# Performance work log

Measured on AMD Instinct MI355X. Metric: run time of the kernel, lower is better.

## Reference

```python
import jax, jax.numpy as jnp
import numpy as np

B, S, D = 2, 2048, 1024
H, HKV, HD = 16, 4, 64
FF = 4096
WINDOW = 1024
EPS = 1e-6


def _rope_tables(seq_len, head_dim, base=10000.0):
    inv_freq = 1.0 / (base ** (np.arange(0, head_dim, 2, dtype=np.float32) / head_dim))
    t = np.arange(seq_len, dtype=np.float32)
    freqs = np.outer(t, inv_freq)                       # [S, HD/2]
    emb = np.concatenate([freqs, freqs], axis=-1)       # [S, HD]
    return jnp.asarray(np.cos(emb)), jnp.asarray(np.sin(emb))


def setup_inputs() -> dict:
    key = jax.random.key(0)
    ks = jax.random.split(key, 16)
    s = lambda fan: 1.0 / np.sqrt(fan)
    cos, sin = _rope_tables(S, HD)
    return {
        "hidden_states": jax.random.normal(ks[0], (B, S, D), jnp.float32),
        "cos": cos, "sin": sin,
        "wq": jax.random.normal(ks[1], (D, H * HD), jnp.float32) * s(D),
        "bq": jnp.zeros((H * HD,), jnp.float32),
        "wk": jax.random.normal(ks[2], (D, HKV * HD), jnp.float32) * s(D),
        "bk": jnp.zeros((HKV * HD,), jnp.float32),
        "wv": jax.random.normal(ks[3], (D, HKV * HD), jnp.float32) * s(D),
        "bv": jnp.zeros((HKV * HD,), jnp.float32),
        "wo": jax.random.normal(ks[4], (H * HD, D), jnp.float32) * s(H * HD),
        "ln1_w": jnp.ones((D,), jnp.float32),
        "ln2_w": jnp.ones((D,), jnp.float32),
        "w_gate": jax.random.normal(ks[5], (D, FF), jnp.float32) * s(D),
        "w_up": jax.random.normal(ks[6], (D, FF), jnp.float32) * s(D),
        "w_down": jax.random.normal(ks[7], (FF, D), jnp.float32) * s(FF),
    }


def _rmsnorm(x, w, eps=EPS):
    var = jnp.mean(x.astype(jnp.float32) ** 2, axis=-1, keepdims=True)
    return (x * jax.lax.rsqrt(var + eps)).astype(x.dtype) * w


def _rotate_half(x):
    x1, x2 = jnp.split(x, 2, axis=-1)
    return jnp.concatenate([-x2, x1], axis=-1)


def reference(hidden_states, cos, sin, wq, bq, wk, bk, wv, bv, wo,
              ln1_w, ln2_w, w_gate, w_up, w_down):
    residual = hidden_states
    h = _rmsnorm(hidden_states, ln1_w)

    # projections -> [B, S, H, HD]
    q = (h @ wq + bq).reshape(B, S, H, HD)
    k = (h @ wk + bk).reshape(B, S, HKV, HD)
    v = (h @ wv + bv).reshape(B, S, HKV, HD)

    # RoPE
    c = cos[None, :, None, :]
    sn = sin[None, :, None, :]
    q = q * c + _rotate_half(q) * sn
    k = k * c + _rotate_half(k) * sn

    # GQA: repeat KV heads to H heads
    groups = H // HKV
    k = jnp.repeat(k, groups, axis=2)  # [B, S, H, HD]
    v = jnp.repeat(v, groups, axis=2)

    # sliding-window causal attention (flex_attention block-mask semantics)
    scale = 1.0 / np.sqrt(HD)
    scores = jnp.einsum("bqhd,bkhd->bhqk", q, k) * scale  # [B, H, S, S]
    i = jnp.arange(S)[:, None]
    j = jnp.arange(S)[None, :]
    mask = (j <= i) & (i - j < WINDOW)
    scores = jnp.where(mask[None, None], scores, jnp.finfo(scores.dtype).min)
    attn = jax.nn.softmax(scores, axis=-1)
    ctx = jnp.einsum("bhqk,bkhd->bqhd", attn, v).reshape(B, S, H * HD)

    h = residual + ctx @ wo

    residual2 = h
    h2 = _rmsnorm(h, ln2_w)
    mlp = (jax.nn.silu(h2 @ w_gate) * (h2 @ w_up)) @ w_down
    return residual2 + mlp
```

## Files before the change

### kernel.cpp

```cpp
#include <hip/hip_runtime.h>
#include <hip/hip_bf16.h>
#include <hip/hip_fp16.h>
#include <math.h>

#define BB 2
#define SS 2048
#define DD 1024
#define HH 16
#define HKVN 4
#define HDIM 64
#define FFD 4096
#define WND 1024
#define EPSF 1e-6f

typedef _Float16 f16;
typedef _Float16 half8 __attribute__((ext_vector_type(8)));
typedef float f32x4 __attribute__((ext_vector_type(4)));
typedef unsigned int u32;

#define GLOAD_LDS(gp, lp)                                                  \
  __builtin_amdgcn_global_load_lds(                                        \
      (const __attribute__((address_space(1))) u32*)(gp),                  \
      (__attribute__((address_space(3))) u32*)(lp), 16, 0, 0)

static __device__ inline u32 pack2(float a, float b) {
  unsigned short ua = __builtin_bit_cast(unsigned short, (f16)a);
  unsigned short ub = __builtin_bit_cast(unsigned short, (f16)b);
  return (u32)ua | ((u32)ub << 16);
}

__global__ __launch_bounds__(256) void prep_weights_kernel(
    const float* __restrict__ wq, const float* __restrict__ wk,
    const float* __restrict__ wv, const float* __restrict__ wo,
    const float* __restrict__ wg, const float* __restrict__ wu,
    const float* __restrict__ wd, const float* __restrict__ bq,
    const float* __restrict__ bk, const float* __restrict__ bv,
    f16* __restrict__ qkvT, f16* __restrict__ woT, f16* __restrict__ wgT,
    f16* __restrict__ wuT, f16* __restrict__ wdT, float* __restrict__ biasC) {
  int t = blockIdx.x;
  if (t >= 3712) {
    int i = (t - 3712) * 256 + threadIdx.x;
    if (i < 1024)
      biasC[i] = bq[i];
    else if (i < 1280)
      biasC[i] = bk[i - 1024];
    else if (i < 1536)
      biasC[i] = bv[i - 1280];
    return;
  }
  const float* W;
  f16* Wt;
  int K, N, lt;
  if (t < 256) {
    W = wq; Wt = qkvT; K = 1024; N = 1024; lt = t;
  } else if (t < 320) {
    W = wk; Wt = qkvT + (size_t)1024 * 1024; K = 1024; N = 256; lt = t - 256;
  } else if (t < 384) {
    W = wv; Wt = qkvT + (size_t)1280 * 1024; K = 1024; N = 256; lt = t - 320;
  } else if (t < 640) {
    W = wo; Wt = woT; K = 1024; N = 1024; lt = t - 384;
  } else if (t < 1664) {
    W = wg; Wt = wgT; K = 1024; N = 4096; lt = t - 640;
  } else if (t < 2688) {
    W = wu; Wt = wuT; K = 1024; N = 4096; lt = t - 1664;
  } else {
    W = wd; Wt = wdT; K = 4096; N = 1024; lt = t - 2688;
  }
  int ntx = N >> 6;
  int n0 = (lt % ntx) * 64, k0 = (lt / ntx) * 64;
  __shared__ float tile[64][65];
  int tx = threadIdx.x & 63, tr = threadIdx.x >> 6;
#pragma unroll
  for (int i = 0; i < 16; i++) {
    int r = tr + i * 4;
    tile[r][tx] = W[(size_t)(k0 + r) * N + n0 + tx];
  }
  __syncthreads();
  int kx = (threadIdx.x & 31) * 2;
  int rr = threadIdx.x >> 5;
#pragma unroll
  for (int i = 0; i < 8; i++) {
    int r = rr + i * 8;
    u32 w = pack2(tile[kx][r], tile[kx + 1][r]);
    *(u32*)(Wt + (size_t)(n0 + r) * K + k0 + kx) = w;
  }
}

__global__ __launch_bounds__(256) void rmsnorm_kernel(
    const float* __restrict__ x, const float* __restrict__ w,
    f16* __restrict__ out) {
  int row = blockIdx.x;
  int tid = threadIdx.x;
  float4 v = ((const float4*)(x + (size_t)row * 1024))[tid];
  float ss = v.x * v.x + v.y * v.y + v.z * v.z + v.w * v.w;
  for (int o = 32; o > 0; o >>= 1) ss += __shfl_down(ss, o, 64);
  __shared__ float red[4];
  int wid = tid >> 6, lane = tid & 63;
  if (lane == 0) red[wid] = ss;
  __syncthreads();
  if (tid == 0)
    red[0] = rsqrtf((red[0] + red[1] + red[2] + red[3]) / 1024.f + EPSF);
  __syncthreads();
  float rs = red[0];
  float4 wv = ((const float4*)w)[tid];
  u32 lo = pack2(v.x * rs * wv.x, v.y * rs * wv.y);
  u32 hi = pack2(v.z * rs * wv.z, v.w * rs * wv.w);
  *(int2*)(out + (size_t)row * 1024 + tid * 4) = make_int2((int)lo, (int)hi);
}

__global__ __launch_bounds__(256) void qkv_gemm(
    const f16* __restrict__ A, const f16* __restrict__ Bt,
    const float* __restrict__ biasC, const float* __restrict__ cos_t,
    const float* __restrict__ sin_t, f16* __restrict__ Qh,
    f16* __restrict__ Kh, f16* __restrict__ Vh, int M, int N, int K) {
  __shared__ __align__(16) char smem[3 * 16384];
  const int tid = threadIdx.x;
  const int lane = tid & 63;
  const int wid = tid >> 6;
  const int wr = wid >> 1, wc = wid & 1;
  const int row0 = blockIdx.y * 128, col0 = blockIdx.x * 128;

  f32x4 acc[4][4];
#pragma unroll
  for (int m = 0; m < 4; m++)
#pragma unroll
    for (int n = 0; n < 4; n++) acc[m][n] = (f32x4){0.f, 0.f, 0.f, 0.f};

  auto stage = [&](int buf, int k0) {
    char* base = smem + buf * 16384;
#pragma unroll
    for (int q = 0; q < 2; q++) {
      int s = wid * 128 + q * 64 + lane;
      int r = s >> 2;
      int cg = (s & 3) ^ ((r >> 1) & 3);
      size_t goff = (size_t)r * K + k0 + cg * 8;
      u32 ldsb = (u32)((wid * 2 + q) * 1024);
      GLOAD_LDS(A + (size_t)row0 * K + goff, base + ldsb);
      GLOAD_LDS(Bt + (size_t)col0 * K + goff, base + 8192 + ldsb);
    }
  };
  auto off = [&](int r, int g) -> int {
    return r * 64 + ((g ^ ((r >> 1) & 3)) << 4);
  };

  const int nt = K / 32;
  stage(0, 0);
  if (nt > 1) stage(1, 32);
  int cur = 0;
  const int g = lane >> 4, l15 = lane & 15;
  for (int t = 0; t < nt; t++) {
    if (t + 1 < nt)
      asm volatile("s_waitcnt vmcnt(4)" ::: "memory");
    else
      asm volatile("s_waitcnt vmcnt(0)" ::: "memory");
    asm volatile("s_waitcnt lgkmcnt(0)" ::: "memory");
    __builtin_amdgcn_sched_barrier(0);
    __builtin_amdgcn_s_barrier();
    __builtin_amdgcn_sched_barrier(0);
    const char* base = smem + cur * 16384;
    half8 af[4], bf[4];
#pragma unroll
    for (int m = 0; m < 4; m++) {
      int r = wr * 64 + m * 16 + l15;
      af[m] = *(const half8*)(base + off(r, g));
    }
#pragma unroll
    for (int n = 0; n < 4; n++) {
      int c = wc * 64 + n * 16 + l15;
      bf[n] = *(const half8*)(base + 8192 + off(c, g));
    }
    if (t + 2 < nt) {
      int nb = cur + 2;
      if (nb >= 3) nb -= 3;
      stage(nb, (t + 2) * 32);
    }
    __builtin_amdgcn_s_setprio(1);
#pragma unroll
    for (int m = 0; m < 4; m++)
#pragma unroll
      for (int n = 0; n < 4; n++)
        acc[m][n] =
            __builtin_amdgcn_mfma_f32_16x16x32_f16(af[m], bf[n], acc[m][n], 0, 0, 0);
    __builtin_amdgcn_s_setprio(0);
    cur = (cur + 1 == 3) ? 0 : cur + 1;
  }

  const int typ = (col0 < 1024) ? 0 : (col0 < 1280 ? 1 : 2);
#pragma unroll
  for (int m = 0; m < 4; m++) {
#pragma unroll
    for (int v = 0; v < 4; v++) {
      int r = row0 + wr * 64 + m * 16 + (lane >> 4) * 4 + v;
      int s = r & (SS - 1);
      if (typ == 2) {
#pragma unroll
        for (int n = 0; n < 4; n++) {
          int c = col0 + wc * 64 + n * 16 + l15;
          float vv = acc[m][n][v] + biasC[c];
          Vh[(size_t)r * 256 + (c - 1280)] = (f16)vv;
        }
      } else {
#pragma unroll
        for (int n = 0; n < 2; n++) {
          int d = n * 16 + l15;
          int c1 = col0 + wc * 64 + d;
          float x1 = acc[m][n][v] + biasC[c1];
          float x2 = acc[m][n + 2][v] + biasC[c1 + 32];
          float cv = cos_t[s * HDIM + d];
          float sv = sin_t[s * HDIM + d];
          float o1 = x1 * cv - x2 * sv;
          float o2 = x2 * cv + x1 * sv;
          if (typ == 0) {
            int h = c1 >> 6;
            f16* qp = Qh + ((size_t)r * HH + h) * HDIM + d;
            qp[0] = (f16)(o1 * 0.125f);
            qp[32] = (f16)(o2 * 0.125f);
          } else {
            int hk = (c1 - 1024) >> 6;
            f16* kp = Kh + ((size_t)r * HKVN + hk) * HDIM + d;
            kp[0] = (f16)o1;
            kp[32] = (f16)o2;
          }
        }
      }
    }
  }
}

__global__ __launch_bounds__(256) void gemm_n64(
    const f16* __restrict__ A, const f16* __restrict__ Bt,
    const float* __restrict__ resid, float* __restrict__ Cf, int M, int N,
    int K) {
  __shared__ __align__(16) char smem[3 * 12288];
  const int tid = threadIdx.x;
  const int lane = tid & 63;
  const int wid = tid >> 6;
  const int wr = wid >> 1, wc = wid & 1;
  const int row0 = blockIdx.y * 128, col0 = blockIdx.x * 64;

  f32x4 acc[4][2];
#pragma unroll
  for (int m = 0; m < 4; m++)
#pragma unroll
    for (int n = 0; n < 2; n++) acc[m][n] = (f32x4){0.f, 0.f, 0.f, 0.f};

  auto stage = [&](int buf, int k0) {
    char* base = smem + buf * 12288;
#pragma unroll
    for (int p = 0; p < 2; p++) {
      int s = p * 256 + tid;
      int r = s >> 2;
      int cg = (s & 3) ^ ((r >> 1) & 3);
      size_t goff = (size_t)r * K + k0 + cg * 8;
      GLOAD_LDS(A + (size_t)row0 * K + goff, base + p * 4096 + wid * 1024);
    }
    {
      int s = tid;
      int r = s >> 2;
      int cg = (s & 3) ^ ((r >> 1) & 3);
      size_t goff = (size_t)r * K + k0 + cg * 8;
      GLOAD_LDS(Bt + (size_t)col0 * K + goff, base + 8192 + wid * 1024);
    }
  };
  auto off = [&](int r, int g) -> int {
    return r * 64 + ((g ^ ((r >> 1) & 3)) << 4);
  };

  const int nt = K / 32;
  stage(0, 0);
  if (nt > 1) stage(1, 32);
  int cur = 0;
  const int g = lane >> 4, l15 = lane & 15;
  for (int t = 0; t < nt; t++) {
    if (t + 1 < nt)
      asm volatile("s_waitcnt vmcnt(3)" ::: "memory");
    else
      asm volatile("s_waitcnt vmcnt(0)" ::: "memory");
    asm volatile("s_waitcnt lgkmcnt(0)" ::: "memory");
    __builtin_amdgcn_sched_barrier(0);
    __builtin_amdgcn_s_barrier();
    __builtin_amdgcn_sched_barrier(0);
    const char* base = smem + cur * 12288;
    half8 af[4], bf[2];
#pragma unroll
    for (int m = 0; m < 4; m++) {
      int r = wr * 64 + m * 16 + l15;
      af[m] = *(const half8*)(base + off(r, g));
    }
#pragma unroll
    for (int n = 0; n < 2; n++) {
      int c = wc * 32 + n * 16 + l15;
      bf[n] = *(const half8*)(base + 8192 + off(c, g));
    }
    if (t + 2 < nt) {
      int nb = cur + 2;
      if (nb >= 3) nb -= 3;
      stage(nb, (t + 2) * 32);
    }
    __builtin_amdgcn_s_setprio(1);
#pragma unroll
    for (int m = 0; m < 4; m++)
#pragma unroll
      for (int n = 0; n < 2; n++)
        acc[m][n] =
            __builtin_amdgcn_mfma_f32_16x16x32_f16(af[m], bf[n], acc[m][n], 0, 0, 0);
    __builtin_amdgcn_s_setprio(0);
    cur = (cur + 1 == 3) ? 0 : cur + 1;
  }

#pragma unroll
  for (int m = 0; m < 4; m++) {
#pragma unroll
    for (int n = 0; n < 2; n++) {
#pragma unroll
      for (int v = 0; v < 4; v++) {
        int r = row0 + wr * 64 + m * 16 + (lane >> 4) * 4 + v;
        int c = col0 + wc * 32 + n * 16 + l15;
        float vv = acc[m][n][v] + resid[(size_t)r * N + c];
        Cf[(size_t)r * N + c] = vv;
      }
    }
  }
}

__global__ __launch_bounds__(512) void gateup_gemm(
    const f16* __restrict__ A, const f16* __restrict__ Wg,
    const f16* __restrict__ Wu, f16* __restrict__ ACT, int M, int N, int K) {
  __shared__ __align__(16) char smem[3 * 40960];
  const int tid = threadIdx.x;
  const int lane = tid & 63;
  const int wid = tid >> 6;
  const int wr = wid >> 2;
  const int wc = wid & 3;
  const int row0 = blockIdx.y * 128, col0 = blockIdx.x * 256;

  f32x4 accg[4][4], accu[4][4];
#pragma unroll
  for (int m = 0; m < 4; m++)
#pragma unroll
    for (int n = 0; n < 4; n++) {
      accg[m][n] = (f32x4){0.f, 0.f, 0.f, 0.f};
      accu[m][n] = (f32x4){0.f, 0.f, 0.f, 0.f};
    }

  auto stage = [&](int buf, int k0) {
    char* base = smem + buf * 40960;
    {
      int s = tid;
      int r = s >> 2;
      int cg = (s & 3) ^ ((r >> 1) & 3);
      size_t goff = (size_t)r * K + k0 + cg * 8;
      GLOAD_LDS(A + (size_t)row0 * K + goff, base + wid * 1024);
    }
#pragma unroll
    for (int p = 0; p < 2; p++) {
      int s = p * 512 + tid;
      int r = s >> 2;
      int cg = (s & 3) ^ ((r >> 1) & 3);
      size_t goff = (size_t)r * K + k0 + cg * 8;
      GLOAD_LDS(Wg + (size_t)col0 * K + goff,
                base + 8192 + p * 8192 + wid * 1024);
    }
#pragma unroll
    for (int p = 0; p < 2; p++) {
      int s = p * 512 + tid;
      int r = s >> 2;
      int cg = (s & 3) ^ ((r >> 1) & 3);
      size_t goff = (size_t)r * K + k0 + cg * 8;
      GLOAD_LDS(Wu + (size_t)col0 * K + goff,
                base + 24576 + p * 8192 + wid * 1024);
    }
  };
  auto off = [&](int r, int g) -> int {
    return r * 64 + ((g ^ ((r >> 1) & 3)) << 4);
  };

  const int nt = K / 32;
  stage(0, 0);
  if (nt > 1) stage(1, 32);
  int cur = 0;
  const int g = lane >> 4, l15 = lane & 15;
  for (int t = 0; t < nt; t++) {
    if (t + 1 < nt)
      asm volatile("s_waitcnt vmcnt(5)" ::: "memory");
    else
      asm volatile("s_waitcnt vmcnt(0)" ::: "memory");
    asm volatile("s_waitcnt lgkmcnt(0)" ::: "memory");
    __builtin_amdgcn_sched_barrier(0);
    __builtin_amdgcn_s_barrier();
    __builtin_amdgcn_sched_barrier(0);
    const char* base = smem + cur * 40960;
    half8 af[4], gf[4], uf[4];
#pragma unroll
    for (int m = 0; m < 4; m++) {
      int r = wr * 64 + m * 16 + l15;
      af[m] = *(const half8*)(base + off(r, g));
    }
#pragma unroll
    for (int n = 0; n < 4; n++) {
      int c = wc * 64 + n * 16 + l15;
      gf[n] = *(const half8*)(base + 8192 + off(c, g));
      uf[n] = *(const half8*)(base + 24576 + off(c, g));
    }
    if (t + 2 < nt) {
      int nb = cur + 2;
      if (nb >= 3) nb -= 3;
      stage(nb, (t + 2) * 32);
    }
    __builtin_amdgcn_s_setprio(1);
#pragma unroll
    for (int m = 0; m < 4; m++)
#pragma unroll
      for (int n = 0; n < 4; n++) {
        accg[m][n] =
            __builtin_amdgcn_mfma_f32_16x16x32_f16(af[m], gf[n], accg[m][n], 0, 0, 0);
        accu[m][n] =
            __builtin_amdgcn_mfma_f32_16x16x32_f16(af[m], uf[n], accu[m][n], 0, 0, 0);
      }
    __builtin_amdgcn_s_setprio(0);
    cur = (cur + 1 == 3) ? 0 : cur + 1;
  }

#pragma unroll
  for (int m = 0; m < 4; m++) {
#pragma unroll
    for (int n = 0; n < 4; n++) {
#pragma unroll
      for (int v = 0; v < 4; v++) {
        int r = row0 + wr * 64 + m * 16 + (lane >> 4) * 4 + v;
        int c = col0 + wc * 64 + n * 16 + l15;
        float gg = accg[m][n][v];
        float uu = accu[m][n][v];
        float sv = gg / (1.f + __expf(-gg));
        ACT[(size_t)r * N + c] = (f16)(sv * uu);
      }
    }
  }
}

__global__ __launch_bounds__(256) void vtrans_kernel(
    const f16* __restrict__ Vh, f16* __restrict__ Vt) {
  __shared__ f16 tile[64][72];
  int st = blockIdx.x & 31;
  int hk = (blockIdx.x >> 5) & 3;
  int b = blockIdx.x >> 7;
  int s0 = st * 64;
  int tid = threadIdx.x;
  int r = tid >> 2, cg = tid & 3;
#pragma unroll
  for (int i = 0; i < 2; i++) {
    const f16* src =
        Vh + (size_t)(b * SS + s0 + r) * 256 + hk * HDIM + cg * 16 + i * 8;
    *(int4*)&tile[r][cg * 16 + i * 8] = *(const int4*)src;
  }
  __syncthreads();
  int dd = tid >> 2, sg = tid & 3;
#pragma unroll
  for (int i = 0; i < 4; i++) {
    int c0 = sg * 16 + i * 4;
    unsigned short a0 = __builtin_bit_cast(unsigned short, tile[c0 + 0][dd]);
    unsigned short a1 = __builtin_bit_cast(unsigned short, tile[c0 + 1][dd]);
    unsigned short a2 = __builtin_bit_cast(unsigned short, tile[c0 + 2][dd]);
    unsigned short a3 = __builtin_bit_cast(unsigned short, tile[c0 + 3][dd]);
    u32 w0 = (u32)a0 | ((u32)a1 << 16);
    u32 w1 = (u32)a2 | ((u32)a3 << 16);
    *(int2*)(Vt + ((size_t)(b * HKVN + hk) * HDIM + dd) * SS + s0 + c0) =
        make_int2((int)w0, (int)w1);
  }
}

__global__ __launch_bounds__(256) void attn_kernel(
    const f16* __restrict__ Qh, const f16* __restrict__ Kh,
    const f16* __restrict__ Vt, f16* __restrict__ O) {
  __shared__ __align__(16) char smem[2 * 16384 + 4 * 4608];
  const int tid = threadIdx.x;
  const int lane = tid & 63;
  const int wid = tid >> 6;
  const int l15 = lane & 15;
  const int g = lane >> 4;
  int qt = blockIdx.x & 63;
  int hk = (blockIdx.x >> 6) & 3;
  int b = blockIdx.x >> 8;
  int s0 = qt * 32;
  int h = hk * 4 + wid;

  half8 qf[2][2];
#pragma unroll
  for (int n = 0; n < 2; n++) {
    int q = s0 + n * 16 + l15;
    const f16* qp = Qh + (((size_t)b * SS + q) * HH + h) * HDIM;
#pragma unroll
    for (int kk = 0; kk < 2; kk++) qf[n][kk] = *(const half8*)(qp + kk * 32 + g * 8);
  }

  const int tb = (s0 >= WND) ? ((s0 - (WND - 1)) >> 6) : 0;
  const int te = (s0 + 31) >> 6;

  f32x4 acc_o[2][4];
#pragma unroll
  for (int m2 = 0; m2 < 2; m2++)
#pragma unroll
    for (int n = 0; n < 4; n++) acc_o[m2][n] = (f32x4){0.f, 0.f, 0.f, 0.f};
  float mrun[2] = {-1e30f, -1e30f};
  float lrun[2] = {0.f, 0.f};

  char* pw = smem + 32768 + wid * 4608;

  auto stage = [&](int buf, int tt) {
    int jt0 = tt * 64;
    char* kbase = smem + buf * 16384;
#pragma unroll
    for (int q2 = 0; q2 < 2; q2++) {
      int slot = (wid * 2 + q2) * 64 + lane;
      int r = slot >> 3, c = slot & 7;
      int cc = c ^ (r & 7);
      u32 ldsb = (u32)((wid * 2 + q2) * 1024);
      const f16* gk =
          Kh + ((size_t)(b * SS + jt0 + r) * HKVN + hk) * HDIM + cc * 8;
      GLOAD_LDS(gk, kbase + ldsb);
      const f16* gv =
          Vt + ((size_t)(b * HKVN + hk) * HDIM + r) * SS + jt0 + cc * 8;
      GLOAD_LDS(gv, kbase + 8192 + ldsb);
    }
  };

  stage(0, tb);
  __syncthreads();
  for (int tt = tb; tt <= te; tt++) {
    int buf = (tt - tb) & 1;
    if (tt < te) stage(buf ^ 1, tt + 1);
    const char* kb = smem + buf * 16384;
    const char* vbp = kb + 8192;
    int jt0 = tt * 64;

    f32x4 acc_s[4][2];
#pragma unroll
    for (int m = 0; m < 4; m++)
#pragma unroll
      for (int n = 0; n < 2; n++) acc_s[m][n] = (f32x4){0.f, 0.f, 0.f, 0.f};
#pragma unroll
    for (int kk = 0; kk < 2; kk++) {
      half8 af[4];
#pragma unroll
      for (int m = 0; m < 4; m++) {
        int key = m * 16 + l15;
        af[m] = *(const half8*)(kb + key * 128 + (((kk * 4 + g) ^ (key & 7)) << 4));
      }
#pragma unroll
      for (int m = 0; m < 4; m++)
#pragma unroll
        for (int n = 0; n < 2; n++)
          acc_s[m][n] = __builtin_amdgcn_mfma_f32_16x16x32_f16(af[m], qf[n][kk],
                                                               acc_s[m][n], 0, 0, 0);
    }

    float tmax[2] = {-1e38f, -1e38f};
#pragma unroll
    for (int m = 0; m < 4; m++)
#pragma unroll
      for (int n = 0; n < 2; n++)
#pragma unroll
        for (int v = 0; v < 4; v++) {
          int j = jt0 + m * 16 + g * 4 + v;
          int q = s0 + n * 16 + l15;
          float s = acc_s[m][n][v];
          s = ((unsigned)(q - j) < (unsigned)WND) ? s : -1e38f;
          acc_s[m][n][v] = s;
          tmax[n] = fmaxf(tmax[n], s);
        }
#pragma unroll
    for (int n = 0; n < 2; n++) {
      tmax[n] = fmaxf(tmax[n], __shfl_xor(tmax[n], 16, 64));
      tmax[n] = fmaxf(tmax[n], __shfl_xor(tmax[n], 32, 64));
    }
    float corr[2], rs[2];
#pragma unroll
    for (int n = 0; n < 2; n++) {
      float mn = fmaxf(mrun[n], tmax[n]);
      corr[n] = __expf(mrun[n] - mn);
      mrun[n] = mn;
      rs[n] = 0.f;
    }
#pragma unroll
    for (int m = 0; m < 4; m++)
#pragma unroll
      for (int n = 0; n < 2; n++) {
        float p0 = __expf(acc_s[m][n][0] - mrun[n]);
        float p1 = __expf(acc_s[m][n][1] - mrun[n]);
        float p2 = __expf(acc_s[m][n][2] - mrun[n]);
        float p3 = __expf(acc_s[m][n][3] - mrun[n]);
        rs[n] += (p0 + p1) + (p2 + p3);
        *(int2*)(pw + (n * 16 + l15) * 144 + (m * 16 + g * 4) * 2) =
            make_int2((int)pack2(p0, p1), (int)pack2(p2, p3));
      }
#pragma unroll
    for (int n = 0; n < 2; n++) {
      rs[n] += __shfl_xor(rs[n], 16, 64);
      rs[n] += __shfl_xor(rs[n], 32, 64);
      lrun[n] = lrun[n] * corr[n] + rs[n];
    }
#pragma unroll
    for (int m2 = 0; m2 < 2; m2++)
#pragma unroll
      for (int v = 0; v < 4; v++) {
        float cw = __shfl(corr[m2], g * 4 + v, 64);
#pragma unroll
        for (int n = 0; n < 4; n++) acc_o[m2][n][v] *= cw;
      }
#pragma unroll
    for (int kk = 0; kk < 2; kk++) {
      half8 ap[2], vf[4];
#pragma unroll
      for (int m2 = 0; m2 < 2; m2++)
        ap[m2] = *(const half8*)(pw + (m2 * 16 + l15) * 144 + (kk * 32 + g * 8) * 2);
#pragma unroll
      for (int n = 0; n < 4; n++) {
        int d = n * 16 + l15;
        vf[n] = *(const half8*)(vbp + d * 128 + (((kk * 4 + g) ^ (d & 7)) << 4));
      }
#pragma unroll
      for (int m2 = 0; m2 < 2; m2++)
#pragma unroll
        for (int n = 0; n < 4; n++)
          acc_o[m2][n] = __builtin_amdgcn_mfma_f32_16x16x32_f16(ap[m2], vf[n],
                                                                acc_o[m2][n], 0, 0, 0);
    }
    __syncthreads();
  }

#pragma unroll
  for (int m2 = 0; m2 < 2; m2++)
#pragma unroll
    for (int v = 0; v < 4; v++) {
      float li = __shfl(lrun[m2], g * 4 + v, 64);
      float inv = 1.f / li;
      int q = s0 + m2 * 16 + g * 4 + v;
#pragma unroll
      for (int n = 0; n < 4; n++) {
        int d = n * 16 + l15;
        O[(((size_t)b * SS + q) * HH + h) * HDIM + d] =
            (f16)(acc_o[m2][n][v] * inv);
      }
    }
}

extern "C" void kernel_launch(void* const* d_in, const int* in_sizes, int n_in,
                              void* d_out, int out_size, void* d_ws,
                              size_t ws_size, hipStream_t stream) {
  const float* hidden = (const float*)d_in[0];
  const float* cos_t = (const float*)d_in[1];
  const float* sin_t = (const float*)d_in[2];
  const float* wq = (const float*)d_in[3];
  const float* bq = (const float*)d_in[4];
  const float* wk = (const float*)d_in[5];
  const float* bk = (const float*)d_in[6];
  const float* wv = (const float*)d_in[7];
  const float* bv = (const float*)d_in[8];
  const float* wo = (const float*)d_in[9];
  const float* ln1 = (const float*)d_in[10];
  const float* ln2 = (const float*)d_in[11];
  const float* wg = (const float*)d_in[12];
  const float* wu = (const float*)d_in[13];
  const float* wd = (const float*)d_in[14];
  float* out = (float*)d_out;
  char* ws = (char*)d_ws;

  const int M = BB * SS;

  f16* qkvT = (f16*)ws;
  f16* woT = (f16*)(ws + (3u << 20));
  f16* wgT = (f16*)(ws + (5u << 20));
  f16* wuT = (f16*)(ws + (13u << 20));
  f16* wdT = (f16*)(ws + (21u << 20));
  f16* Anh = (f16*)(ws + (29u << 20));
  f16* CTXh = (f16*)(ws + (37u << 20));
  f16* Vh = (f16*)(ws + (45u << 20));
  f16* Qh = (f16*)(ws + (57u << 20));
  f16* Kh = (f16*)(ws + (65u << 20));
  f16* Vt = (f16*)(ws + (67u << 20));
  f16* ACTh = (f16*)(ws + (45u << 20));
  float* biasC = (float*)(ws + (81u << 20));

  prep_weights_kernel<<<3718, 256, 0, stream>>>(wq, wk, wv, wo, wg, wu, wd, bq,
                                                bk, bv, qkvT, woT, wgT, wuT,
                                                wdT, biasC);
  rmsnorm_kernel<<<M, 256, 0, stream>>>(hidden, ln1, Anh);
  qkv_gemm<<<dim3(1536 / 128, M / 128), 256, 0, stream>>>(
      Anh, qkvT, biasC, cos_t, sin_t, Qh, Kh, Vh, M, 1536, DD);
  vtrans_kernel<<<BB * HKVN * (SS / 64), 256, 0, stream>>>(Vh, Vt);
  attn_kernel<<<BB * HKVN * (SS / 32), 256, 0, stream>>>(Qh, Kh, Vt, CTXh);
  gemm_n64<<<dim3(DD / 64, M / 128), 256, 0, stream>>>(CTXh, woT, hidden, out,
                                                       M, DD, DD);
  rmsnorm_kernel<<<M, 256, 0, stream>>>(out, ln2, Anh);
  gateup_gemm<<<dim3(FFD / 256, M / 128), 512, 0, stream>>>(Anh, wgT, wuT, ACTh,
                                                            M, FFD, DD);
  gemm_n64<<<dim3(DD / 64, M / 128), 256, 0, stream>>>(ACTh, wdT, out, out, M,
                                                       DD, FFD);
}
```

Measured before the change: 253.0 us.

## Interleave gate/up weights and use 256x256 tiled gate-up GEMM with 8-wave pipeline

Weight prep now writes the gate and up weight rows interleaved into one combined matrix, so the gate-up projection becomes a single GEMM with N=8192. The new kernel uses 256x256 output tiles with K-steps of 64, double-buffered LDS split into A and B halves, and staggered async global-to-LDS loads placed between MFMA groups. SiLU(gate)*up is computed in the epilogue by exchanging neighbouring lanes with a shuffle. The aim is higher arithmetic intensity per LDS byte and better overlap of loads with MFMAs. In exchange it uses 128KB of LDS, keeps 128 accumulator registers per thread, and has complex hand-placed wait counts that are easy to get wrong.

After: 269.4 us. 6.5% more time.

```diff
diff --git a/kernel.cpp b/kernel.cpp
--- a/kernel.cpp
+++ b/kernel.cpp
@@ -35,8 +35,8 @@
     const float* __restrict__ wg, const float* __restrict__ wu,
     const float* __restrict__ wd, const float* __restrict__ bq,
     const float* __restrict__ bk, const float* __restrict__ bv,
-    f16* __restrict__ qkvT, f16* __restrict__ woT, f16* __restrict__ wgT,
-    f16* __restrict__ wuT, f16* __restrict__ wdT, float* __restrict__ biasC) {
+    f16* __restrict__ qkvT, f16* __restrict__ woT, f16* __restrict__ Wi,
+    f16* __restrict__ wdT, float* __restrict__ biasC) {
   int t = blockIdx.x;
   if (t >= 3712) {
     int i = (t - 3712) * 256 + threadIdx.x;
@@ -50,7 +50,7 @@
   }
   const float* W;
   f16* Wt;
-  int K, N, lt;
+  int K, N, lt, rmul = 1, radd = 0;
   if (t < 256) {
     W = wq; Wt = qkvT; K = 1024; N = 1024; lt = t;
   } else if (t < 320) {
@@ -60,9 +60,9 @@
   } else if (t < 640) {
     W = wo; Wt = woT; K = 1024; N = 1024; lt = t - 384;
   } else if (t < 1664) {
-    W = wg; Wt = wgT; K = 1024; N = 4096; lt = t - 640;
+    W = wg; Wt = Wi; K = 1024; N = 4096; lt = t - 640; rmul = 2; radd = 0;
   } else if (t < 2688) {
-    W = wu; Wt = wuT; K = 1024; N = 4096; lt = t - 1664;
+    W = wu; Wt = Wi; K = 1024; N = 4096; lt = t - 1664; rmul = 2; radd = 1;
   } else {
     W = wd; Wt = wdT; K = 4096; N = 1024; lt = t - 2688;
   }
@@ -82,7 +82,7 @@
   for (int i = 0; i < 8; i++) {
     int r = rr + i * 8;
     u32 w = pack2(tile[kx][r], tile[kx + 1][r]);
-    *(u32*)(Wt + (size_t)(n0 + r) * K + k0 + kx) = w;
+    *(u32*)(Wt + ((size_t)((n0 + r) * rmul + radd)) * K + k0 + kx) = w;
   }
 }
 
@@ -323,116 +323,130 @@
   }
 }
 
-__global__ __launch_bounds__(512) void gateup_gemm(
-    const f16* __restrict__ A, const f16* __restrict__ Wg,
-    const f16* __restrict__ Wu, f16* __restrict__ ACT, int M, int N, int K) {
-  __shared__ __align__(16) char smem[3 * 40960];
+__global__ __launch_bounds__(512) void gateup_gemm8(
+    const f16* __restrict__ A, const f16* __restrict__ Wi,
+    f16* __restrict__ ACT, int M) {
+  __shared__ __align__(16) char smem[2 * 65536];
   const int tid = threadIdx.x;
   const int lane = tid & 63;
   const int wid = tid >> 6;
   const int wr = wid >> 2;
   const int wc = wid & 3;
-  const int row0 = blockIdx.y * 128, col0 = blockIdx.x * 256;
-
-  f32x4 accg[4][4], accu[4][4];
-#pragma unroll
-  for (int m = 0; m < 4; m++)
+  const int l15 = lane & 15, g = lane >> 4;
+  const int row0 = blockIdx.y * 256, col0 = blockIdx.x * 256;
+  const int K = 1024;
+
+  f32x4 acc[8][4];
+#pragma unroll
+  for (int m = 0; m < 8; m++)
+#pragma unroll
+    for (int n = 0; n < 4; n++) acc[m][n] = (f32x4){0.f, 0.f, 0.f, 0.f};
+
+  const f16* Ap = A + (size_t)row0 * K;
+  const f16* Bp = Wi + (size_t)col0 * K;
+
+  auto stage = [&](const f16* src, char* dstbase, int kt) {
+    int k0 = kt * 64;
+#pragma unroll
+    for (int p = 0; p < 4; p++) {
+      int slot = p * 512 + tid;
+      int r = slot >> 3, c = slot & 7;
+      int cc = c ^ (r & 7);
+      GLOAD_LDS(src + (size_t)r * K + k0 + cc * 8,
+                dstbase + p * 8192 + wid * 1024);
+    }
+  };
+
+  stage(Ap, smem, 0);
+  stage(Bp, smem + 32768, 0);
+  stage(Bp, smem + 65536 + 32768, 1);
+  asm volatile("s_waitcnt vmcnt(4)" ::: "memory");
+  __builtin_amdgcn_sched_barrier(0);
+  __builtin_amdgcn_s_barrier();
+  __builtin_amdgcn_sched_barrier(0);
+
+  for (int i = 0; i < 8; i++) {
+    const bool last = (i == 7);
+#pragma unroll
+    for (int half = 0; half < 2; half++) {
+      const char* tb = smem + half * 65536;
+      half8 bf[4][2];
+#pragma unroll
+      for (int q = 0; q < 4; q++) {
+        int m0 = 2 * q, m1 = 2 * q + 1;
+        int r0 = wr * 128 + m0 * 16 + l15;
+        int r1 = wr * 128 + m1 * 16 + l15;
+        half8 a0 = *(const half8*)(tb + r0 * 128 + ((g ^ (r0 & 7)) << 4));
+        half8 a1 = *(const half8*)(tb + r0 * 128 + (((4 + g) ^ (r0 & 7)) << 4));
+        half8 a2 = *(const half8*)(tb + r1 * 128 + ((g ^ (r1 & 7)) << 4));
+        half8 a3 = *(const half8*)(tb + r1 * 128 + (((4 + g) ^ (r1 & 7)) << 4));
+        if (q == 0) {
+#pragma unroll
+          for (int n = 0; n < 4; n++) {
+            int rb = wc * 64 + n * 16 + l15;
+            bf[n][0] =
+                *(const half8*)(tb + 32768 + rb * 128 + ((g ^ (rb & 7)) << 4));
+            bf[n][1] = *(const half8*)(tb + 32768 + rb * 128 +
+                                       (((4 + g) ^ (rb & 7)) << 4));
+          }
+        }
+        if (half == 0) {
+          if (q == 0) stage(Ap, smem + 65536, 2 * i + 1);
+          if (q == 2 && !last) stage(Bp, smem + 32768, 2 * i + 2);
+        } else {
+          if (q == 0 && !last) stage(Ap, smem, 2 * i + 2);
+          if (q == 2 && !last)
+            stage(Bp, smem + 65536 + 32768, 2 * i + 3);
+        }
+        __builtin_amdgcn_sched_barrier(0);
+        __builtin_amdgcn_s_barrier();
+        asm volatile("s_waitcnt lgkmcnt(0)" ::: "memory");
+        __builtin_amdgcn_sched_barrier(0);
+        __builtin_amdgcn_s_setprio(1);
+#pragma unroll
+        for (int n = 0; n < 4; n++) {
+          acc[m0][n] =
+              __builtin_amdgcn_mfma_f32_16x16x32_f16(a0, bf[n][0], acc[m0][n], 0, 0, 0);
+          acc[m0][n] =
+              __builtin_amdgcn_mfma_f32_16x16x32_f16(a1, bf[n][1], acc[m0][n], 0, 0, 0);
+          acc[m1][n] =
+              __builtin_amdgcn_mfma_f32_16x16x32_f16(a2, bf[n][0], acc[m1][n], 0, 0, 0);
+          acc[m1][n] =
+              __builtin_amdgcn_mfma_f32_16x16x32_f16(a3, bf[n][1], acc[m1][n], 0, 0, 0);
+        }
+        __builtin_amdgcn_s_setprio(0);
+        if (q == 3) {
+          if (half == 0) {
+            if (last)
+              asm volatile("s_waitcnt vmcnt(0)" ::: "memory");
+            else
+              asm volatile("s_waitcnt vmcnt(4)" ::: "memory");
+          } else if (!last) {
+            asm volatile("s_waitcnt vmcnt(4)" ::: "memory");
+          }
+        }
+        __builtin_amdgcn_sched_barrier(0);
+        __builtin_amdgcn_s_barrier();
+        __builtin_amdgcn_sched_barrier(0);
+      }
+    }
+  }
+
+  const int col0h = col0 >> 1;
+#pragma unroll
+  for (int m = 0; m < 8; m++) {
 #pragma unroll
     for (int n = 0; n < 4; n++) {
-      accg[m][n] = (f32x4){0.f, 0.f, 0.f, 0.f};
-      accu[m][n] = (f32x4){0.f, 0.f, 0.f, 0.f};
-    }
-
-  auto stage = [&](int buf, int k0) {
-    char* base = smem + buf * 40960;
-    {
-      int s = tid;
-      int r = s >> 2;
-      int cg = (s & 3) ^ ((r >> 1) & 3);
-      size_t goff = (size_t)r * K + k0 + cg * 8;
-      GLOAD_LDS(A + (size_t)row0 * K + goff, base + wid * 1024);
-    }
-#pragma unroll
-    for (int p = 0; p < 2; p++) {
-      int s = p * 512 + tid;
-      int r = s >> 2;
-      int cg = (s & 3) ^ ((r >> 1) & 3);
-      size_t goff = (size_t)r * K + k0 + cg * 8;
-      GLOAD_LDS(Wg + (size_t)col0 * K + goff,
-                base + 8192 + p * 8192 + wid * 1024);
-    }
-#pragma unroll
-    for (int p = 0; p < 2; p++) {
-      int s = p * 512 + tid;
-      int r = s >> 2;
-      int cg = (s & 3) ^ ((r >> 1) & 3);
-      size_t goff = (size_t)r * K + k0 + cg * 8;
-      GLOAD_LDS(Wu + (size_t)col0 * K + goff,
-                base + 24576 + p * 8192 + wid * 1024);
-    }
-  };
-  auto off = [&](int r, int g) -> int {
-    return r * 64 + ((g ^ ((r >> 1) & 3)) << 4);
-  };
-
-  const int nt = K / 32;
-  stage(0, 0);
-  if (nt > 1) stage(1, 32);
-  int cur = 0;
-  const int g = lane >> 4, l15 = lane & 15;
-  for (int t = 0; t < nt; t++) {
-    if (t + 1 < nt)
-      asm volatile("s_waitcnt vmcnt(5)" ::: "memory");
-    else
-      asm volatile("s_waitcnt vmcnt(0)" ::: "memory");
-    asm volatile("s_waitcnt lgkmcnt(0)" ::: "memory");
-    __builtin_amdgcn_sched_barrier(0);
-    __builtin_amdgcn_s_barrier();
-    __builtin_amdgcn_sched_barrier(0);
-    const char* base = smem + cur * 40960;
-    half8 af[4], gf[4], uf[4];
-#pragma unroll
-    for (int m = 0; m < 4; m++) {
-      int r = wr * 64 + m * 16 + l15;
-      af[m] = *(const half8*)(base + off(r, g));
-    }
-#pragma unroll
-    for (int n = 0; n < 4; n++) {
-      int c = wc * 64 + n * 16 + l15;
-      gf[n] = *(const half8*)(base + 8192 + off(c, g));
-      uf[n] = *(const half8*)(base + 24576 + off(c, g));
-    }
-    if (t + 2 < nt) {
-      int nb = cur + 2;
-      if (nb >= 3) nb -= 3;
-      stage(nb, (t + 2) * 32);
-    }
-    __builtin_amdgcn_s_setprio(1);
-#pragma unroll
-    for (int m = 0; m < 4; m++)
-#pragma unroll
-      for (int n = 0; n < 4; n++) {
-        accg[m][n] =
-            __builtin_amdgcn_mfma_f32_16x16x32_f16(af[m], gf[n], accg[m][n], 0, 0, 0);
-        accu[m][n] =
-            __builtin_amdgcn_mfma_f32_16x16x32_f16(af[m], uf[n], accu[m][n], 0, 0, 0);
-      }
-    __builtin_amdgcn_s_setprio(0);
-    cur = (cur + 1 == 3) ? 0 : cur + 1;
-  }
-
-#pragma unroll
-  for (int m = 0; m < 4; m++) {
-#pragma unroll
-    for (int n = 0; n < 4; n++) {
 #pragma unroll
       for (int v = 0; v < 4; v++) {
-        int r = row0 + wr * 64 + m * 16 + (lane >> 4) * 4 + v;
-        int c = col0 + wc * 64 + n * 16 + l15;
-        float gg = accg[m][n][v];
-        float uu = accu[m][n][v];
-        float sv = gg / (1.f + __expf(-gg));
-        ACT[(size_t)r * N + c] = (f16)(sv * uu);
+        float other = __shfl_xor(acc[m][n][v], 1, 64);
+        if (!(l15 & 1)) {
+          float gg = acc[m][n][v];
+          float sv = gg / (1.f + __expf(-gg));
+          int r = row0 + wr * 128 + m * 16 + g * 4 + v;
+          int c = col0h + wc * 32 + n * 8 + (l15 >> 1);
+          ACT[(size_t)r * FFD + c] = (f16)(sv * other);
+        }
       }
     }
   }
@@ -669,8 +683,7 @@
 
   f16* qkvT = (f16*)ws;
   f16* woT = (f16*)(ws + (3u << 20));
-  f16* wgT = (f16*)(ws + (5u << 20));
-  f16* wuT = (f16*)(ws + (13u << 20));
+  f16* Wi = (f16*)(ws + (5u << 20));
   f16* wdT = (f16*)(ws + (21u << 20));
   f16* Anh = (f16*)(ws + (29u << 20));
   f16* CTXh = (f16*)(ws + (37u << 20));
@@ -682,8 +695,8 @@
   float* biasC = (float*)(ws + (81u << 20));
 
   prep_weights_kernel<<<3718, 256, 0, stream>>>(wq, wk, wv, wo, wg, wu, wd, bq,
-                                                bk, bv, qkvT, woT, wgT, wuT,
-                                                wdT, biasC);
+                                                bk, bv, qkvT, woT, Wi, wdT,
+                                                biasC);
   rmsnorm_kernel<<<M, 256, 0, stream>>>(hidden, ln1, Anh);
   qkv_gemm<<<dim3(1536 / 128, M / 128), 256, 0, stream>>>(
       Anh, qkvT, biasC, cos_t, sin_t, Qh, Kh, Vh, M, 1536, DD);
@@ -692,8 +705,8 @@
   gemm_n64<<<dim3(DD / 64, M / 128), 256, 0, stream>>>(CTXh, woT, hidden, out,
                                                        M, DD, DD);
   rmsnorm_kernel<<<M, 256, 0, stream>>>(out, ln2, Anh);
-  gateup_gemm<<<dim3(FFD / 256, M / 128), 512, 0, stream>>>(Anh, wgT, wuT, ACTh,
-                                                            M, FFD, DD);
+  gateup_gemm8<<<dim3(2 * FFD / 256, M / 256), 512, 0, stream>>>(Anh, Wi, ACTh,
+                                                                 M);
   gemm_n64<<<dim3(DD / 64, M / 128), 256, 0, stream>>>(ACTh, wdT, out, out, M,
                                                        DD, FFD);
 }
```
